# Performance work log

Hardware: AMD Instinct MI355X
Metric: run time of the kernel (lower is better)

Reference implementation:

```python
import jax, jax.numpy as jnp
import numpy as np

DIM = 256
NUM_HEADS = 4
HEAD_DIM = DIM // NUM_HEADS
MLP_HIDDEN = int(DIM * 2.0)
SCALE = HEAD_DIM ** -0.5
LN_EPS = 1e-5


def _layernorm(x, gamma, beta):
    mu = jnp.mean(x, axis=-1, keepdims=True)
    var = jnp.mean(jnp.square(x - mu), axis=-1, keepdims=True)
    return (x - mu) * jax.lax.rsqrt(var + LN_EPS) * gamma + beta


def setup_inputs() -> dict:
    key = jax.random.key(0)
    ks = jax.random.split(key, 8)
    B, C, N, P = 8, DIM, 64, 256
    s = 0.02
    return {
        "x": jax.random.normal(ks[0], (B, C, N, P), dtype=jnp.float32),
        # torch Linear weights stored [out_features, in_features]
        "W_qkv": jax.random.normal(ks[1], (3 * DIM, DIM), dtype=jnp.float32) * s,
        "W_proj": jax.random.normal(ks[2], (DIM, DIM), dtype=jnp.float32) * s,
        "b_proj": jnp.zeros((DIM,), dtype=jnp.float32),
        "ln1_g": jnp.ones((DIM,), dtype=jnp.float32),
        "ln1_b": jnp.zeros((DIM,), dtype=jnp.float32),
        "ln2_g": jnp.ones((DIM,), dtype=jnp.float32),
        "ln2_b": jnp.zeros((DIM,), dtype=jnp.float32),
        "W_mlp1": jax.random.normal(ks[3], (MLP_HIDDEN, DIM), dtype=jnp.float32) * s,
        "b_mlp1": jnp.zeros((MLP_HIDDEN,), dtype=jnp.float32),
        "W_mlp2": jax.random.normal(ks[4], (DIM, MLP_HIDDEN), dtype=jnp.float32) * s,
        "b_mlp2": jnp.zeros((DIM,), dtype=jnp.float32),
    }


def reference(x, W_qkv, W_proj, b_proj, ln1_g, ln1_b, ln2_g, ln2_b,
              W_mlp1, b_mlp1, W_mlp2, b_mlp2):
    B, C, N, P = x.shape
    H, D = NUM_HEADS, HEAD_DIM
    # [B,C,N,P] -> [B*N, P, C]
    x_seq = jnp.transpose(x, (0, 2, 3, 1)).reshape(B * N, P, C)
    shortcut = x_seq

    h = _layernorm(x_seq, ln1_g, ln1_b)
    qkv = jnp.einsum('spc,oc->spo', h, W_qkv)              # [BN, P, 3C]
    qkv = qkv.reshape(B * N, P, 3, H, D)
    q = jnp.transpose(qkv[:, :, 0], (0, 2, 1, 3))          # [BN, H, P, D]
    k = jnp.transpose(qkv[:, :, 1], (0, 2, 1, 3))
    v = jnp.transpose(qkv[:, :, 2], (0, 2, 1, 3))

    attn = jnp.einsum('shpd,shqd->shpq', q, k) * SCALE     # [BN, H, P, P]
    attn = jax.nn.softmax(attn, axis=-1)
    o = jnp.einsum('shpq,shqd->shpd', attn, v)             # [BN, H, P, D]
    o = jnp.transpose(o, (0, 2, 1, 3)).reshape(B * N, P, C)
    o = jnp.einsum('spc,oc->spo', o, W_proj) + b_proj

    x_seq = shortcut + o

    h2 = _layernorm(x_seq, ln2_g, ln2_b)
    m = jnp.einsum('spc,oc->spo', h2, W_mlp1) + b_mlp1
    m = jax.nn.gelu(m, approximate=False)
    m = jnp.einsum('sph,oh->spo', m, W_mlp2) + b_mlp2
    x_seq = x_seq + m

    out = x_seq.reshape(B, N, P, C)
    return jnp.transpose(out, (0, 3, 1, 2))                # [B, C, N, P]
```

## Files before the change

### kernel.cpp

```cpp
#include <hip/hip_runtime.h>
#include <stdint.h>
#include <math.h>


#define DEV static __device__ __forceinline__

typedef __bf16 bf16x8 __attribute__((ext_vector_type(8)));
typedef float  f32x4  __attribute__((ext_vector_type(4)));

union B8 { bf16x8 v; uint4 q; uint32_t u[4]; uint16_t h[8]; };

DEV uint16_t f2bf(float f) {
  uint32_t u = __float_as_uint(f);
  return (uint16_t)((u + 0x7FFFu + ((u >> 16) & 1u)) >> 16);
}
DEV float bf2f(uint16_t h) { return __uint_as_float(((uint32_t)h) << 16); }
DEV uint32_t pk2(float a, float b) { return (uint32_t)f2bf(a) | ((uint32_t)f2bf(b) << 16); }

DEV f32x4 mfma16(const B8& a, const B8& b, f32x4 c) {
  return __builtin_amdgcn_mfma_f32_16x16x32_bf16(a.v, b.v, c, 0, 0, 0);
}

DEV uint32_t shfl_u(uint32_t v, int src) { return (uint32_t)__shfl((int)v, src, 64); }

DEV B8 mk(const uint32_t* w) {
  B8 x; x.u[0] = w[0]; x.u[1] = w[1]; x.u[2] = w[2]; x.u[3] = w[3]; return x;
}

DEV void xpose(const uint32_t* pk0, const uint32_t* pk1, int kd, int g, int r, uint32_t* out) {
  const int sA = 32 * (g & 1) + r;
  const int sB = sA + 16;
  const int tA = 2 * kd, tB = 2 * kd + 1;
  uint32_t a0 = shfl_u(pk0[tA], sA), b0 = shfl_u(pk0[tB], sA);
  uint32_t a1 = shfl_u(pk1[tA], sA), b1 = shfl_u(pk1[tB], sA);
  uint32_t a2 = shfl_u(pk0[tA], sB), b2 = shfl_u(pk0[tB], sB);
  uint32_t a3 = shfl_u(pk1[tA], sB), b3 = shfl_u(pk1[tB], sB);
  const bool hi = g >= 2;
  out[0] = hi ? b0 : a0;
  out[1] = hi ? b1 : a1;
  out[2] = hi ? b2 : a2;
  out[3] = hi ? b3 : a3;
}

__global__ void transformer_prep(const float* __restrict__ wqkv,
                                 const float* __restrict__ wproj,
                                 const float* __restrict__ w1,
                                 const float* __restrict__ w2,
                                 uint16_t* __restrict__ wbf) {
  int e = blockIdx.x * 256 + threadIdx.x;
  float v;
  if (e < 196608)      v = wqkv[e] * (e < 65536 ? 0.18033688011112042f : 1.0f);
  else if (e < 262144) v = wproj[e - 196608];
  else if (e < 393216) v = w1[e - 262144];
  else                 v = w2[e - 393216];
  wbf[e] = f2bf(v);
}

__global__ __launch_bounds__(512, 2) void transformer_k1(
    const float* __restrict__ x,
    const float* __restrict__ bproj,
    const float* __restrict__ ln1g, const float* __restrict__ ln1b,
    const float* __restrict__ ln2g, const float* __restrict__ ln2b,
    const uint16_t* __restrict__ wbf,
    uint16_t* __restrict__ h2,
    float* __restrict__ out) {
  __shared__ __attribute__((aligned(16))) uint8_t lds[163840];
  const int tid = threadIdx.x;
  const int lane = tid & 63;
  const int wv = tid >> 6;
  const int r = lane & 15;
  const int g = lane >> 4;
  const int s = blockIdx.x;
  const int bb = s >> 6, nn = s & 63;
  const float* xs = x + (size_t)bb * 4194304 + (size_t)nn * 256;
  float* outp = out + (size_t)bb * 4194304 + (size_t)nn * 256;
  const f32x4 fz = {0.f, 0.f, 0.f, 0.f};

  uint32_t hfrag[2][8][4];
  float s1[2] = {0.f, 0.f}, s2[2] = {0.f, 0.f};
#pragma unroll
  for (int ch = 0; ch < 4; ++ch) {
#pragma unroll
    for (int i = 0; i < 8; ++i) {
      int f = i * 512 + tid;
      int c = f >> 6;
      int p4 = (f & 63) << 2;
      f32x4 v = *(const f32x4*)(xs + (size_t)(ch * 64 + c) * 16384 + p4);
      *(f32x4*)(lds + (c * 264 + p4) * 4) = v;
    }
    __syncthreads();
#pragma unroll
    for (int rt = 0; rt < 2; ++rt) {
      int p = 32 * wv + 16 * rt + r;
#pragma unroll
      for (int ktl = 0; ktl < 2; ++ktl) {
        int cl0 = 32 * ktl + 8 * g;
        float v[8];
#pragma unroll
        for (int j = 0; j < 8; ++j) {
          v[j] = *(const float*)(lds + ((cl0 + j) * 264 + p) * 4);
          s1[rt] += v[j];
          s2[rt] += v[j] * v[j];
        }
#pragma unroll
        for (int w = 0; w < 4; ++w) hfrag[rt][2 * ch + ktl][w] = pk2(v[2 * w], v[2 * w + 1]);
      }
    }
    __syncthreads();
  }
  float mu[2], rs[2];
#pragma unroll
  for (int rt = 0; rt < 2; ++rt) {
    float a = s1[rt]; a += __shfl_xor(a, 16, 64); a += __shfl_xor(a, 32, 64);
    float b = s2[rt]; b += __shfl_xor(b, 16, 64); b += __shfl_xor(b, 32, 64);
    mu[rt] = a * (1.0f / 256.0f);
    float var = b * (1.0f / 256.0f) - mu[rt] * mu[rt];
    rs[rt] = rsqrtf(var + 1e-5f);
  }
#pragma unroll
  for (int kt = 0; kt < 8; ++kt) {
    int c0 = 32 * kt + 8 * g;
    f32x4 gA = *(const f32x4*)(ln1g + c0), gB = *(const f32x4*)(ln1g + c0 + 4);
    f32x4 bA = *(const f32x4*)(ln1b + c0), bB = *(const f32x4*)(ln1b + c0 + 4);
#pragma unroll
    for (int rt = 0; rt < 2; ++rt) {
#pragma unroll
      for (int w = 0; w < 4; ++w) {
        uint32_t pw = hfrag[rt][kt][w];
        float lo = bf2f((uint16_t)(pw & 0xFFFFu));
        float hi = bf2f((uint16_t)(pw >> 16));
        float glo = (w < 2) ? gA[2 * w] : gB[2 * w - 4];
        float ghi = (w < 2) ? gA[2 * w + 1] : gB[2 * w - 3];
        float blo = (w < 2) ? bA[2 * w] : bB[2 * w - 4];
        float bhi = (w < 2) ? bA[2 * w + 1] : bB[2 * w - 3];
        lo = (lo - mu[rt]) * rs[rt] * glo + blo;
        hi = (hi - mu[rt]) * rs[rt] * ghi + bhi;
        hfrag[rt][kt][w] = pk2(lo, hi);
      }
    }
  }
  __syncthreads();

  uint32_t oa[2][8][4];
#pragma unroll
  for (int hd = 0; hd < 4; ++hd) {
#pragma unroll
    for (int m = 0; m < 3; ++m) {
      const uint16_t* src = wbf + (m * 256 + hd * 64) * 256;
#pragma unroll
      for (int i = 0; i < 4; ++i) {
        int f = i * 512 + tid;
        int row = f >> 5, c16 = f & 31;
        uint4 v = *(const uint4*)(src + row * 256 + c16 * 8);
        *(uint4*)(lds + ((65536 + m * 32768 + row * 512 + c16 * 16) ^ ((row & 7) << 4))) = v;
      }
    }
    __syncthreads();

#pragma unroll
    for (int m = 0; m < 2; ++m) {
      const int wb_base = 65536 + (m + 1) * 32768;
      f32x4 acc[2][4];
#pragma unroll
      for (int rt = 0; rt < 2; ++rt)
#pragma unroll
        for (int ct = 0; ct < 4; ++ct) acc[rt][ct] = fz;
#pragma unroll
      for (int kt = 0; kt < 8; ++kt) {
#pragma unroll
        for (int ct = 0; ct < 4; ++ct) {
          B8 wfr;
          wfr.q = *(const uint4*)(lds + ((wb_base + (16 * ct + r) * 512 + (32 * kt + 8 * g) * 2) ^ ((r & 7) << 4)));
#pragma unroll
          for (int rt = 0; rt < 2; ++rt) {
            B8 a = mk(hfrag[rt][kt]);
            acc[rt][ct] = mfma16(a, wfr, acc[rt][ct]);
          }
        }
      }
#pragma unroll
      for (int rt = 0; rt < 2; ++rt) {
#pragma unroll
        for (int ct = 0; ct < 4; ++ct) {
          int d = 16 * ct + r;
          int q0 = 32 * wv + 16 * rt + 4 * g;
          if (m == 0) {
#pragma unroll
            for (int i = 0; i < 4; ++i) {
              int qq = q0 + i;
              *(uint16_t*)(lds + ((qq * 128 + d * 2) ^ ((qq & 7) << 4))) = f2bf(acc[rt][ct][i]);
            }
          } else {
            uint2 pv;
            pv.x = pk2(acc[rt][ct][0], acc[rt][ct][1]);
            pv.y = pk2(acc[rt][ct][2], acc[rt][ct][3]);
            *(uint2*)(lds + ((32768 + d * 512 + q0 * 2) ^ ((d & 7) << 4))) = pv;
          }
        }
      }
    }
    __syncthreads();

#pragma unroll
    for (int pt = 0; pt < 2; ++pt) {
      f32x4 qT[4];
#pragma unroll
      for (int mt = 0; mt < 4; ++mt) qT[mt] = fz;
#pragma unroll
      for (int kt = 0; kt < 8; ++kt) {
        B8 hb = mk(hfrag[pt][kt]);
#pragma unroll
        for (int mt = 0; mt < 4; ++mt) {
          B8 wa;
          wa.q = *(const uint4*)(lds + ((65536 + (16 * mt + r) * 512 + (32 * kt + 8 * g) * 2) ^ ((r & 7) << 4)));
          qT[mt] = mfma16(wa, hb, qT[mt]);
        }
      }
      uint32_t pq0[4], pq1[4];
#pragma unroll
      for (int mt = 0; mt < 4; ++mt) {
        pq0[mt] = pk2(qT[mt][0], qT[mt][1]);
        pq1[mt] = pk2(qT[mt][2], qT[mt][3]);
      }
      uint32_t qb[2][4];
#pragma unroll
      for (int kd = 0; kd < 2; ++kd) xpose(pq0, pq1, kd, g, r, qb[kd]);

      float m_ = -1e30f, l_ = 0.f;
      f32x4 oT[4];
#pragma unroll
      for (int dt = 0; dt < 4; ++dt) oT[dt] = fz;

#pragma unroll 1
      for (int chk = 0; chk < 4; ++chk) {
        f32x4 sT[4];
#pragma unroll
        for (int qt = 0; qt < 4; ++qt) sT[qt] = fz;
#pragma unroll
        for (int kd = 0; kd < 2; ++kd) {
          B8 qf = mk(qb[kd]);
#pragma unroll
          for (int qt = 0; qt < 4; ++qt) {
            int qq = chk * 64 + 16 * qt + r;
            B8 ka;
            ka.q = *(const uint4*)(lds + ((qq * 128 + (32 * kd + 8 * g) * 2) ^ ((qq & 7) << 4)));
            sT[qt] = mfma16(ka, qf, sT[qt]);
          }
        }
        float tmax = sT[0][0];
#pragma unroll
        for (int qt = 0; qt < 4; ++qt)
#pragma unroll
          for (int i = 0; i < 4; ++i) tmax = fmaxf(tmax, sT[qt][i]);
        tmax = fmaxf(tmax, __shfl_xor(tmax, 16, 64));
        tmax = fmaxf(tmax, __shfl_xor(tmax, 32, 64));
        float mn = fmaxf(m_, tmax);
        float fcor = exp2f(m_ - mn);
        float ts = 0.f;
#pragma unroll
        for (int qt = 0; qt < 4; ++qt)
#pragma unroll
          for (int i = 0; i < 4; ++i) {
            float e = exp2f(sT[qt][i] - mn);
            sT[qt][i] = e;
            ts += e;
          }
        ts += __shfl_xor(ts, 16, 64);
        ts += __shfl_xor(ts, 32, 64);
        l_ = l_ * fcor + ts;
        m_ = mn;
#pragma unroll
        for (int dt = 0; dt < 4; ++dt)
#pragma unroll
          for (int i = 0; i < 4; ++i) oT[dt][i] *= fcor;
        uint32_t pp0[4], pp1[4];
#pragma unroll
        for (int qt = 0; qt < 4; ++qt) {
          pp0[qt] = pk2(sT[qt][0], sT[qt][1]);
          pp1[qt] = pk2(sT[qt][2], sT[qt][3]);
        }
#pragma unroll
        for (int qk = 0; qk < 2; ++qk) {
          uint32_t pb[4];
          xpose(pp0, pp1, qk, g, r, pb);
          B8 pf = mk(pb);
#pragma unroll
          for (int dt = 0; dt < 4; ++dt) {
            B8 va;
            va.q = *(const uint4*)(lds + ((32768 + (16 * dt + r) * 512 + (chk * 64 + 32 * qk + 8 * g) * 2) ^ ((r & 7) << 4)));
            oT[dt] = mfma16(va, pf, oT[dt]);
          }
        }
      }
      float inv = 1.0f / l_;
      uint32_t po0[4], po1[4];
#pragma unroll
      for (int dt = 0; dt < 4; ++dt) {
        po0[dt] = pk2(oT[dt][0] * inv, oT[dt][1] * inv);
        po1[dt] = pk2(oT[dt][2] * inv, oT[dt][3] * inv);
      }
#pragma unroll
      for (int kd = 0; kd < 2; ++kd) xpose(po0, po1, kd, g, r, oa[pt][2 * hd + kd]);
    }
    __syncthreads();
  }

  const uint16_t* wp = wbf + 196608;
  float s1r[2][4], s2r[2][4];
#pragma unroll
  for (int rt = 0; rt < 2; ++rt)
#pragma unroll
    for (int i = 0; i < 4; ++i) { s1r[rt][i] = 0.f; s2r[rt][i] = 0.f; }
#pragma unroll 1
  for (int q3 = 0; q3 < 4; ++q3) {
#pragma unroll
    for (int i = 0; i < 4; ++i) {
      int f = i * 512 + tid;
      int row = f >> 5, c16 = f & 31;
      uint4 v = *(const uint4*)(wp + (q3 * 64 + row) * 256 + c16 * 8);
      *(uint4*)(lds + ((131072 + row * 512 + c16 * 16) ^ ((row & 7) << 4))) = v;
    }
    __syncthreads();
    f32x4 acc[2][4];
#pragma unroll
    for (int rt = 0; rt < 2; ++rt)
#pragma unroll
      for (int ct = 0; ct < 4; ++ct) acc[rt][ct] = fz;
#pragma unroll
    for (int kt = 0; kt < 8; ++kt) {
#pragma unroll
      for (int ct = 0; ct < 4; ++ct) {
        B8 wfr;
        wfr.q = *(const uint4*)(lds + ((131072 + (16 * ct + r) * 512 + (32 * kt + 8 * g) * 2) ^ ((r & 7) << 4)));
#pragma unroll
        for (int rt = 0; rt < 2; ++rt) {
          B8 a = mk(oa[rt][kt]);
          acc[rt][ct] = mfma16(a, wfr, acc[rt][ct]);
        }
      }
    }
#pragma unroll
    for (int rt = 0; rt < 2; ++rt) {
#pragma unroll
      for (int ct = 0; ct < 4; ++ct) {
        int c = q3 * 64 + 16 * ct + r;
        float bias = bproj[c];
        int p0 = 32 * wv + 16 * rt + 4 * g;
        f32x4 res = *(const f32x4*)(xs + (size_t)c * 16384 + p0);
        f32x4 x2v;
#pragma unroll
        for (int i = 0; i < 4; ++i) x2v[i] = acc[rt][ct][i] + bias + res[i];
        *(f32x4*)(outp + (size_t)c * 16384 + p0) = x2v;
#pragma unroll
        for (int i = 0; i < 4; ++i) {
          s1r[rt][i] += x2v[i];
          s2r[rt][i] += x2v[i] * x2v[i];
          int pp = p0 + i;
          *(uint16_t*)(lds + ((pp * 512 + c * 2) ^ ((pp & 7) << 4))) = f2bf(x2v[i]);
        }
      }
    }
    __syncthreads();
  }
#pragma unroll
  for (int rt = 0; rt < 2; ++rt)
#pragma unroll
    for (int i = 0; i < 4; ++i) {
      float a = s1r[rt][i], b = s2r[rt][i];
#pragma unroll
      for (int off = 1; off < 16; off <<= 1) {
        a += __shfl_xor(a, off, 64);
        b += __shfl_xor(b, off, 64);
      }
      float m = a * (1.0f / 256.0f);
      float var = b * (1.0f / 256.0f) - m * m;
      s1r[rt][i] = m;
      s2r[rt][i] = rsqrtf(var + 1e-5f);
    }
  if (r == 0) {
#pragma unroll
    for (int rt = 0; rt < 2; ++rt)
#pragma unroll
      for (int i = 0; i < 4; ++i) {
        int pp = 32 * wv + 16 * rt + 4 * g + i;
        float2 st; st.x = s1r[rt][i]; st.y = s2r[rt][i];
        *(float2*)(lds + 131072 + pp * 8) = st;
      }
  }
  __syncthreads();
  {
    int pp = tid >> 1;
    int chf = tid & 1;
    float2 st = *(const float2*)(lds + 131072 + pp * 8);
#pragma unroll
    for (int kk = 0; kk < 16; ++kk) {
      int c0 = chf * 128 + kk * 8;
      B8 xv;
      xv.q = *(const uint4*)(lds + ((pp * 512 + c0 * 2) ^ ((pp & 7) << 4)));
      f32x4 gA = *(const f32x4*)(ln2g + c0), gB = *(const f32x4*)(ln2g + c0 + 4);
      f32x4 bA = *(const f32x4*)(ln2b + c0), bB = *(const f32x4*)(ln2b + c0 + 4);
      B8 ov;
#pragma unroll
      for (int j = 0; j < 8; ++j) {
        float v = bf2f(xv.h[j]);
        float gg = (j < 4) ? gA[j & 3] : gB[j & 3];
        float bb2 = (j < 4) ? bA[j & 3] : bB[j & 3];
        v = (v - st.x) * st.y * gg + bb2;
        ov.h[j] = f2bf(v);
      }
      *(uint4*)(h2 + (size_t)s * 65536 + pp * 256 + c0) = ov.q;
    }
  }
}

__global__ __launch_bounds__(512, 2) void transformer_k2(
    const uint16_t* __restrict__ h2,
    const uint16_t* __restrict__ w1,
    const uint16_t* __restrict__ w2,
    const float* __restrict__ bm1,
    const float* __restrict__ bm2,
    float* __restrict__ out) {
  __shared__ __attribute__((aligned(16))) uint8_t lds[98304];
  const int tid = threadIdx.x;
  const int lane = tid & 63;
  const int wv = tid >> 6;
  const int r = lane & 15, g = lane >> 4;
  const int bid = blockIdx.x;
  const int s = bid >> 2, tg = bid & 3;
  const int bb = s >> 6, nn = s & 63;
  const f32x4 fz = {0.f, 0.f, 0.f, 0.f};

#pragma unroll
  for (int i = 0; i < 4; ++i) {
    int f = i * 512 + tid;
    int row = f >> 5, c16 = f & 31;
    uint4 v = *(const uint4*)(h2 + (size_t)s * 65536 + (tg * 64 + row) * 256 + c16 * 8);
    *(uint4*)(lds + ((row * 512 + c16 * 16) ^ ((row & 7) << 4))) = v;
  }
  __syncthreads();

  f32x4 acc[4][4];
#pragma unroll
  for (int mt = 0; mt < 4; ++mt)
#pragma unroll
    for (int nt = 0; nt < 4; ++nt) acc[mt][nt] = fz;
#pragma unroll
  for (int kt = 0; kt < 8; ++kt) {
    B8 a[4];
#pragma unroll
    for (int mt = 0; mt < 4; ++mt)
      a[mt].q = *(const uint4*)(lds + (((16 * mt + r) * 512 + (32 * kt + 8 * g) * 2) ^ ((r & 7) << 4)));
#pragma unroll
    for (int nt = 0; nt < 4; ++nt) {
      B8 bfr;
      bfr.q = *(const uint4*)(w1 + ((64 * wv + 16 * nt + r) * 256 + 32 * kt + 8 * g));
#pragma unroll
      for (int mt = 0; mt < 4; ++mt) acc[mt][nt] = mfma16(a[mt], bfr, acc[mt][nt]);
    }
  }
#pragma unroll
  for (int nt = 0; nt < 4; ++nt) {
    int n = 64 * wv + 16 * nt + r;
    float bias = bm1[n];
#pragma unroll
    for (int mt = 0; mt < 4; ++mt) {
#pragma unroll
      for (int i = 0; i < 4; ++i) {
        float v = acc[mt][nt][i] + bias;
        v = 0.5f * v * (1.0f + erff(v * 0.70710678118654752440f));
        int row = 16 * mt + 4 * g + i;
        *(uint16_t*)(lds + ((32768 + row * 1024 + n * 2) ^ ((row & 7) << 4))) = f2bf(v);
      }
    }
  }
  __syncthreads();

  f32x4 acc2[4][2];
#pragma unroll
  for (int mt = 0; mt < 4; ++mt)
#pragma unroll
    for (int nt = 0; nt < 2; ++nt) acc2[mt][nt] = fz;
#pragma unroll
  for (int kt = 0; kt < 16; ++kt) {
    B8 a[4];
#pragma unroll
    for (int mt = 0; mt < 4; ++mt)
      a[mt].q = *(const uint4*)(lds + ((32768 + (16 * mt + r) * 1024 + (32 * kt + 8 * g) * 2) ^ ((r & 7) << 4)));
#pragma unroll
    for (int nt = 0; nt < 2; ++nt) {
      B8 bfr;
      bfr.q = *(const uint4*)(w2 + ((32 * wv + 16 * nt + r) * 512 + 32 * kt + 8 * g));
#pragma unroll
      for (int mt = 0; mt < 4; ++mt) acc2[mt][nt] = mfma16(a[mt], bfr, acc2[mt][nt]);
    }
  }
  float* outp = out + (size_t)bb * 4194304 + (size_t)nn * 256;
#pragma unroll
  for (int nt = 0; nt < 2; ++nt) {
    int c = 32 * wv + 16 * nt + r;
    float bias = bm2[c];
#pragma unroll
    for (int mt = 0; mt < 4; ++mt) {
      int p0 = tg * 64 + 16 * mt + 4 * g;
      f32x4 v = *(const f32x4*)(outp + (size_t)c * 16384 + p0);
#pragma unroll
      for (int i = 0; i < 4; ++i) v[i] += acc2[mt][nt][i] + bias;
      *(f32x4*)(outp + (size_t)c * 16384 + p0) = v;
    }
  }
}

extern "C" void kernel_launch(void* const* d_in, const int* in_sizes, int n_in,
                              void* d_out, int out_size, void* d_ws, size_t ws_size,
                              hipStream_t stream) {
  (void)in_sizes; (void)n_in; (void)out_size; (void)ws_size;
  const float* x     = (const float*)d_in[0];
  const float* wqkv  = (const float*)d_in[1];
  const float* wproj = (const float*)d_in[2];
  const float* bproj = (const float*)d_in[3];
  const float* ln1g  = (const float*)d_in[4];
  const float* ln1b  = (const float*)d_in[5];
  const float* ln2g  = (const float*)d_in[6];
  const float* ln2b  = (const float*)d_in[7];
  const float* w1    = (const float*)d_in[8];
  const float* bm1   = (const float*)d_in[9];
  const float* w2    = (const float*)d_in[10];
  const float* bm2   = (const float*)d_in[11];
  uint16_t* wbf = (uint16_t*)d_ws;
  uint16_t* h2  = wbf + 524288;
  float* out = (float*)d_out;

  transformer_prep<<<2048, 256, 0, stream>>>(wqkv, wproj, w1, w2, wbf);
  transformer_k1<<<512, 512, 0, stream>>>(x, bproj, ln1g, ln1b, ln2g, ln2b, wbf, h2, out);
  transformer_k2<<<2048, 512, 0, stream>>>(h2, wbf + 262144, wbf + 393216, bm1, bm2, out);
}
```

Baseline: 779.7 us.

## Pre-swizzle weights into MFMA fragment order, shrink LDS, move LN2 into MLP kernel

The prep kernel now writes bf16 weights in MFMA fragment-tiled order, so both kernels read weight fragments straight from global memory instead of staging them through LDS. Kernel 1 drops from 160KB to 64KB of LDS with launch bounds raised to 4 blocks, reads x directly from global, and spills attention output fragments to a workspace instead of holding them in registers. LayerNorm2 moves from kernel 1 into kernel 2, which recomputes statistics from the residual stream it reads back. The MLP is split into two hidden halves to cut register and LDS use. The cost is more global traffic: strided uncoalesced x reads, repeated weight fragment loads from cache, and an extra osc round trip.

After: 1.049 ms. +34.6%, slower.

```diff
diff --git a/kernel.cpp b/kernel.cpp
--- a/kernel.cpp
+++ b/kernel.cpp
@@ -46,25 +46,31 @@
                                  const float* __restrict__ wproj,
                                  const float* __restrict__ w1,
                                  const float* __restrict__ w2,
-                                 uint16_t* __restrict__ wbf) {
+                                 uint16_t* __restrict__ dst) {
   int e = blockIdx.x * 256 + threadIdx.x;
-  float v;
-  if (e < 196608)      v = wqkv[e] * (e < 65536 ? 0.18033688011112042f : 1.0f);
-  else if (e < 262144) v = wproj[e - 196608];
-  else if (e < 393216) v = w1[e - 262144];
-  else                 v = w2[e - 393216];
-  wbf[e] = f2bf(v);
-}
-
-__global__ __launch_bounds__(512, 2) void transformer_k1(
+  const float* src; int C, local;
+  if (e < 196608)      { src = wqkv;  C = 256; local = e; }
+  else if (e < 262144) { src = wproj; C = 256; local = e - 196608; }
+  else if (e < 393216) { src = w1;    C = 256; local = e - 262144; }
+  else                 { src = w2;    C = 512; local = e - 393216; }
+  int k32 = C >> 5;
+  int tile = local >> 9, within = local & 511;
+  int ln = within >> 3, j = within & 7;
+  int tr = tile / k32, tk = tile - tr * k32;
+  int row = tr * 16 + (ln & 15), col = tk * 32 + (ln >> 4) * 8 + j;
+  float v = src[row * C + col];
+  if (e < 65536) v *= 0.18033688011112042f;
+  dst[e] = f2bf(v);
+}
+
+__global__ __launch_bounds__(512, 4) void transformer_k1(
     const float* __restrict__ x,
     const float* __restrict__ bproj,
     const float* __restrict__ ln1g, const float* __restrict__ ln1b,
-    const float* __restrict__ ln2g, const float* __restrict__ ln2b,
-    const uint16_t* __restrict__ wbf,
-    uint16_t* __restrict__ h2,
+    const uint16_t* __restrict__ wf,
+    uint16_t* __restrict__ osc,
     float* __restrict__ out) {
-  __shared__ __attribute__((aligned(16))) uint8_t lds[163840];
+  __shared__ __attribute__((aligned(16))) uint8_t lds[65536];
   const int tid = threadIdx.x;
   const int lane = tid & 63;
   const int wv = tid >> 6;
@@ -79,34 +85,21 @@
   uint32_t hfrag[2][8][4];
   float s1[2] = {0.f, 0.f}, s2[2] = {0.f, 0.f};
 #pragma unroll
-  for (int ch = 0; ch < 4; ++ch) {
-#pragma unroll
-    for (int i = 0; i < 8; ++i) {
-      int f = i * 512 + tid;
-      int c = f >> 6;
-      int p4 = (f & 63) << 2;
-      f32x4 v = *(const f32x4*)(xs + (size_t)(ch * 64 + c) * 16384 + p4);
-      *(f32x4*)(lds + (c * 264 + p4) * 4) = v;
-    }
-    __syncthreads();
-#pragma unroll
-    for (int rt = 0; rt < 2; ++rt) {
-      int p = 32 * wv + 16 * rt + r;
-#pragma unroll
-      for (int ktl = 0; ktl < 2; ++ktl) {
-        int cl0 = 32 * ktl + 8 * g;
-        float v[8];
-#pragma unroll
-        for (int j = 0; j < 8; ++j) {
-          v[j] = *(const float*)(lds + ((cl0 + j) * 264 + p) * 4);
-          s1[rt] += v[j];
-          s2[rt] += v[j] * v[j];
-        }
-#pragma unroll
-        for (int w = 0; w < 4; ++w) hfrag[rt][2 * ch + ktl][w] = pk2(v[2 * w], v[2 * w + 1]);
-      }
-    }
-    __syncthreads();
+  for (int rt = 0; rt < 2; ++rt) {
+    int p = 32 * wv + 16 * rt + r;
+#pragma unroll
+    for (int kt = 0; kt < 8; ++kt) {
+      int c0 = 32 * kt + 8 * g;
+      float v[8];
+#pragma unroll
+      for (int j = 0; j < 8; ++j) {
+        v[j] = xs[(size_t)(c0 + j) * 16384 + p];
+        s1[rt] += v[j];
+        s2[rt] += v[j] * v[j];
+      }
+#pragma unroll
+      for (int w = 0; w < 4; ++w) hfrag[rt][kt][w] = pk2(v[2 * w], v[2 * w + 1]);
+    }
   }
   float mu[2], rs[2];
 #pragma unroll
@@ -139,27 +132,11 @@
       }
     }
   }
-  __syncthreads();
-
-  uint32_t oa[2][8][4];
-#pragma unroll
+
+#pragma unroll 1
   for (int hd = 0; hd < 4; ++hd) {
 #pragma unroll
-    for (int m = 0; m < 3; ++m) {
-      const uint16_t* src = wbf + (m * 256 + hd * 64) * 256;
-#pragma unroll
-      for (int i = 0; i < 4; ++i) {
-        int f = i * 512 + tid;
-        int row = f >> 5, c16 = f & 31;
-        uint4 v = *(const uint4*)(src + row * 256 + c16 * 8);
-        *(uint4*)(lds + ((65536 + m * 32768 + row * 512 + c16 * 16) ^ ((row & 7) << 4))) = v;
-      }
-    }
-    __syncthreads();
-
-#pragma unroll
     for (int m = 0; m < 2; ++m) {
-      const int wb_base = 65536 + (m + 1) * 32768;
       f32x4 acc[2][4];
 #pragma unroll
       for (int rt = 0; rt < 2; ++rt)
@@ -170,7 +147,7 @@
 #pragma unroll
         for (int ct = 0; ct < 4; ++ct) {
           B8 wfr;
-          wfr.q = *(const uint4*)(lds + ((wb_base + (16 * ct + r) * 512 + (32 * kt + 8 * g) * 2) ^ ((r & 7) << 4)));
+          wfr.q = *(const uint4*)(wf + (size_t)((((m + 1) * 16 + hd * 4 + ct) * 8 + kt) * 512) + lane * 8);
 #pragma unroll
           for (int rt = 0; rt < 2; ++rt) {
             B8 a = mk(hfrag[rt][kt]);
@@ -201,7 +178,7 @@
     }
     __syncthreads();
 
-#pragma unroll
+#pragma unroll 1
     for (int pt = 0; pt < 2; ++pt) {
       f32x4 qT[4];
 #pragma unroll
@@ -212,7 +189,7 @@
 #pragma unroll
         for (int mt = 0; mt < 4; ++mt) {
           B8 wa;
-          wa.q = *(const uint4*)(lds + ((65536 + (16 * mt + r) * 512 + (32 * kt + 8 * g) * 2) ^ ((r & 7) << 4)));
+          wa.q = *(const uint4*)(wf + (size_t)(((hd * 4 + mt) * 8 + kt) * 512) + lane * 8);
           qT[mt] = mfma16(wa, hb, qT[mt]);
         }
       }
@@ -300,27 +277,18 @@
         po1[dt] = pk2(oT[dt][2] * inv, oT[dt][3] * inv);
       }
 #pragma unroll
-      for (int kd = 0; kd < 2; ++kd) xpose(po0, po1, kd, g, r, oa[pt][2 * hd + kd]);
+      for (int kd = 0; kd < 2; ++kd) {
+        uint32_t ofr[4];
+        xpose(po0, po1, kd, g, r, ofr);
+        B8 t; t.u[0] = ofr[0]; t.u[1] = ofr[1]; t.u[2] = ofr[2]; t.u[3] = ofr[3];
+        *(uint4*)(osc + (size_t)((s * 16 + 2 * wv + pt) * 8 + 2 * hd + kd) * 512 + lane * 8) = t.q;
+      }
     }
     __syncthreads();
   }
 
-  const uint16_t* wp = wbf + 196608;
-  float s1r[2][4], s2r[2][4];
-#pragma unroll
-  for (int rt = 0; rt < 2; ++rt)
-#pragma unroll
-    for (int i = 0; i < 4; ++i) { s1r[rt][i] = 0.f; s2r[rt][i] = 0.f; }
 #pragma unroll 1
   for (int q3 = 0; q3 < 4; ++q3) {
-#pragma unroll
-    for (int i = 0; i < 4; ++i) {
-      int f = i * 512 + tid;
-      int row = f >> 5, c16 = f & 31;
-      uint4 v = *(const uint4*)(wp + (q3 * 64 + row) * 256 + c16 * 8);
-      *(uint4*)(lds + ((131072 + row * 512 + c16 * 16) ^ ((row & 7) << 4))) = v;
-    }
-    __syncthreads();
     f32x4 acc[2][4];
 #pragma unroll
     for (int rt = 0; rt < 2; ++rt)
@@ -328,15 +296,16 @@
       for (int ct = 0; ct < 4; ++ct) acc[rt][ct] = fz;
 #pragma unroll
     for (int kt = 0; kt < 8; ++kt) {
+      B8 a[2];
+#pragma unroll
+      for (int rt = 0; rt < 2; ++rt)
+        a[rt].q = *(const uint4*)(osc + (size_t)((s * 16 + 2 * wv + rt) * 8 + kt) * 512 + lane * 8);
 #pragma unroll
       for (int ct = 0; ct < 4; ++ct) {
         B8 wfr;
-        wfr.q = *(const uint4*)(lds + ((131072 + (16 * ct + r) * 512 + (32 * kt + 8 * g) * 2) ^ ((r & 7) << 4)));
-#pragma unroll
-        for (int rt = 0; rt < 2; ++rt) {
-          B8 a = mk(oa[rt][kt]);
-          acc[rt][ct] = mfma16(a, wfr, acc[rt][ct]);
-        }
+        wfr.q = *(const uint4*)(wf + 196608 + (size_t)(((q3 * 4 + ct) * 8 + kt) * 512) + lane * 8);
+#pragma unroll
+        for (int rt = 0; rt < 2; ++rt) acc[rt][ct] = mfma16(a[rt], wfr, acc[rt][ct]);
       }
     }
 #pragma unroll
@@ -351,76 +320,17 @@
 #pragma unroll
         for (int i = 0; i < 4; ++i) x2v[i] = acc[rt][ct][i] + bias + res[i];
         *(f32x4*)(outp + (size_t)c * 16384 + p0) = x2v;
-#pragma unroll
-        for (int i = 0; i < 4; ++i) {
-          s1r[rt][i] += x2v[i];
-          s2r[rt][i] += x2v[i] * x2v[i];
-          int pp = p0 + i;
-          *(uint16_t*)(lds + ((pp * 512 + c * 2) ^ ((pp & 7) << 4))) = f2bf(x2v[i]);
-        }
-      }
-    }
-    __syncthreads();
-  }
-#pragma unroll
-  for (int rt = 0; rt < 2; ++rt)
-#pragma unroll
-    for (int i = 0; i < 4; ++i) {
-      float a = s1r[rt][i], b = s2r[rt][i];
-#pragma unroll
-      for (int off = 1; off < 16; off <<= 1) {
-        a += __shfl_xor(a, off, 64);
-        b += __shfl_xor(b, off, 64);
-      }
-      float m = a * (1.0f / 256.0f);
-      float var = b * (1.0f / 256.0f) - m * m;
-      s1r[rt][i] = m;
-      s2r[rt][i] = rsqrtf(var + 1e-5f);
-    }
-  if (r == 0) {
-#pragma unroll
-    for (int rt = 0; rt < 2; ++rt)
-#pragma unroll
-      for (int i = 0; i < 4; ++i) {
-        int pp = 32 * wv + 16 * rt + 4 * g + i;
-        float2 st; st.x = s1r[rt][i]; st.y = s2r[rt][i];
-        *(float2*)(lds + 131072 + pp * 8) = st;
-      }
-  }
-  __syncthreads();
-  {
-    int pp = tid >> 1;
-    int chf = tid & 1;
-    float2 st = *(const float2*)(lds + 131072 + pp * 8);
-#pragma unroll
-    for (int kk = 0; kk < 16; ++kk) {
-      int c0 = chf * 128 + kk * 8;
-      B8 xv;
-      xv.q = *(const uint4*)(lds + ((pp * 512 + c0 * 2) ^ ((pp & 7) << 4)));
-      f32x4 gA = *(const f32x4*)(ln2g + c0), gB = *(const f32x4*)(ln2g + c0 + 4);
-      f32x4 bA = *(const f32x4*)(ln2b + c0), bB = *(const f32x4*)(ln2b + c0 + 4);
-      B8 ov;
-#pragma unroll
-      for (int j = 0; j < 8; ++j) {
-        float v = bf2f(xv.h[j]);
-        float gg = (j < 4) ? gA[j & 3] : gB[j & 3];
-        float bb2 = (j < 4) ? bA[j & 3] : bB[j & 3];
-        v = (v - st.x) * st.y * gg + bb2;
-        ov.h[j] = f2bf(v);
-      }
-      *(uint4*)(h2 + (size_t)s * 65536 + pp * 256 + c0) = ov.q;
-    }
-  }
-}
-
-__global__ __launch_bounds__(512, 2) void transformer_k2(
-    const uint16_t* __restrict__ h2,
-    const uint16_t* __restrict__ w1,
-    const uint16_t* __restrict__ w2,
-    const float* __restrict__ bm1,
-    const float* __restrict__ bm2,
+      }
+    }
+  }
+}
+
+__global__ __launch_bounds__(512, 4) void transformer_k2(
+    const float* __restrict__ ln2g, const float* __restrict__ ln2b,
+    const uint16_t* __restrict__ w1f, const uint16_t* __restrict__ w2f,
+    const float* __restrict__ bm1, const float* __restrict__ bm2,
     float* __restrict__ out) {
-  __shared__ __attribute__((aligned(16))) uint8_t lds[98304];
+  __shared__ __attribute__((aligned(16))) uint8_t lds[68608];
   const int tid = threadIdx.x;
   const int lane = tid & 63;
   const int wv = tid >> 6;
@@ -428,84 +338,135 @@
   const int bid = blockIdx.x;
   const int s = bid >> 2, tg = bid & 3;
   const int bb = s >> 6, nn = s & 63;
+  float* outp = out + (size_t)bb * 4194304 + (size_t)nn * 256;
+  const int tokbase = tg * 64;
   const f32x4 fz = {0.f, 0.f, 0.f, 0.f};
-
-#pragma unroll
-  for (int i = 0; i < 4; ++i) {
-    int f = i * 512 + tid;
-    int row = f >> 5, c16 = f & 31;
-    uint4 v = *(const uint4*)(h2 + (size_t)s * 65536 + (tg * 64 + row) * 256 + c16 * 8);
-    *(uint4*)(lds + ((row * 512 + c16 * 16) ^ ((row & 7) << 4))) = v;
+  const int mtw = wv & 3, kth = wv >> 2;
+  const int p = tokbase + 16 * mtw + r;
+
+  float v[4][8];
+  float s1 = 0.f, s2 = 0.f;
+#pragma unroll
+  for (int k2l = 0; k2l < 4; ++k2l) {
+    int c0 = (kth * 4 + k2l) * 32 + 8 * g;
+#pragma unroll
+    for (int j = 0; j < 8; ++j) {
+      float t = outp[(size_t)(c0 + j) * 16384 + p];
+      v[k2l][j] = t;
+      s1 += t;
+      s2 += t * t;
+    }
+  }
+  s1 += __shfl_xor(s1, 16, 64); s1 += __shfl_xor(s1, 32, 64);
+  s2 += __shfl_xor(s2, 16, 64); s2 += __shfl_xor(s2, 32, 64);
+  if (g == 0) {
+    float2 pr; pr.x = s1; pr.y = s2;
+    *(float2*)(lds + 65536 + ((16 * mtw + r) * 2 + kth) * 8) = pr;
   }
   __syncthreads();
-
-  f32x4 acc[4][4];
+  if (tid < 64) {
+    float2 a = *(const float2*)(lds + 65536 + (tid * 2 + 0) * 8);
+    float2 b = *(const float2*)(lds + 65536 + (tid * 2 + 1) * 8);
+    float su = a.x + b.x, sq = a.y + b.y;
+    float m = su * (1.0f / 256.0f);
+    float var = sq * (1.0f / 256.0f) - m * m;
+    float2 st; st.x = m; st.y = rsqrtf(var + 1e-5f);
+    *(float2*)(lds + 66560 + tid * 8) = st;
+  }
+  __syncthreads();
+  float2 st = *(const float2*)(lds + 66560 + (16 * mtw + r) * 8);
+#pragma unroll
+  for (int k2l = 0; k2l < 4; ++k2l) {
+    int kt = kth * 4 + k2l;
+    int c0 = kt * 32 + 8 * g;
+    f32x4 gA = *(const f32x4*)(ln2g + c0), gB = *(const f32x4*)(ln2g + c0 + 4);
+    f32x4 bA = *(const f32x4*)(ln2b + c0), bB = *(const f32x4*)(ln2b + c0 + 4);
+    float nv[8];
+#pragma unroll
+    for (int j = 0; j < 8; ++j) {
+      float gg = (j < 4) ? gA[j] : gB[j - 4];
+      float bb2 = (j < 4) ? bA[j] : bB[j - 4];
+      nv[j] = (v[k2l][j] - st.x) * st.y * gg + bb2;
+    }
+    B8 t;
+#pragma unroll
+    for (int w = 0; w < 4; ++w) t.u[w] = pk2(nv[2 * w], nv[2 * w + 1]);
+    *(uint4*)(lds + (mtw * 8 + kt) * 1024 + lane * 16) = t.q;
+  }
+  __syncthreads();
+
+  f32x4 acc2[4][2];
 #pragma unroll
   for (int mt = 0; mt < 4; ++mt)
 #pragma unroll
-    for (int nt = 0; nt < 4; ++nt) acc[mt][nt] = fz;
-#pragma unroll
-  for (int kt = 0; kt < 8; ++kt) {
-    B8 a[4];
+    for (int nt = 0; nt < 2; ++nt) acc2[mt][nt] = fz;
+
+#pragma unroll 1
+  for (int half = 0; half < 2; ++half) {
+    f32x4 acc1[4][2];
 #pragma unroll
     for (int mt = 0; mt < 4; ++mt)
-      a[mt].q = *(const uint4*)(lds + (((16 * mt + r) * 512 + (32 * kt + 8 * g) * 2) ^ ((r & 7) << 4)));
-#pragma unroll
-    for (int nt = 0; nt < 4; ++nt) {
-      B8 bfr;
-      bfr.q = *(const uint4*)(w1 + ((64 * wv + 16 * nt + r) * 256 + 32 * kt + 8 * g));
-#pragma unroll
-      for (int mt = 0; mt < 4; ++mt) acc[mt][nt] = mfma16(a[mt], bfr, acc[mt][nt]);
-    }
-  }
-#pragma unroll
-  for (int nt = 0; nt < 4; ++nt) {
-    int n = 64 * wv + 16 * nt + r;
-    float bias = bm1[n];
+#pragma unroll
+      for (int nt = 0; nt < 2; ++nt) acc1[mt][nt] = fz;
+#pragma unroll
+    for (int kt = 0; kt < 8; ++kt) {
+      B8 a[4];
+#pragma unroll
+      for (int mt = 0; mt < 4; ++mt)
+        a[mt].q = *(const uint4*)(lds + (mt * 8 + kt) * 1024 + lane * 16);
+#pragma unroll
+      for (int nt = 0; nt < 2; ++nt) {
+        B8 bfr;
+        bfr.q = *(const uint4*)(w1f + (size_t)((((half * 16 + wv * 2 + nt) * 8) + kt) * 512) + lane * 8);
+#pragma unroll
+        for (int mt = 0; mt < 4; ++mt) acc1[mt][nt] = mfma16(a[mt], bfr, acc1[mt][nt]);
+      }
+    }
+    if (half) __syncthreads();
+#pragma unroll
+    for (int nt = 0; nt < 2; ++nt) {
+      int nl = wv * 32 + 16 * nt + r;
+      float bias = bm1[half * 256 + nl];
+#pragma unroll
+      for (int mt = 0; mt < 4; ++mt) {
+#pragma unroll
+        for (int i = 0; i < 4; ++i) {
+          float vv = acc1[mt][nt][i] + bias;
+          vv = 0.5f * vv * (1.0f + erff(vv * 0.70710678118654752440f));
+          int lp = (4 * g + i) + 16 * ((nl >> 3) & 3);
+          *(uint16_t*)(lds + 32768 + (mt * 8 + wv) * 1024 + lp * 16 + (nl & 7) * 2) = f2bf(vv);
+        }
+      }
+    }
+    __syncthreads();
+#pragma unroll
+    for (int kt = 0; kt < 8; ++kt) {
+      B8 a[4];
+#pragma unroll
+      for (int mt = 0; mt < 4; ++mt)
+        a[mt].q = *(const uint4*)(lds + 32768 + (mt * 8 + kt) * 1024 + lane * 16);
+#pragma unroll
+      for (int nt = 0; nt < 2; ++nt) {
+        B8 bfr;
+        bfr.q = *(const uint4*)(w2f + (size_t)(((wv * 2 + nt) * 16 + half * 8 + kt) * 512) + lane * 8);
+#pragma unroll
+        for (int mt = 0; mt < 4; ++mt) acc2[mt][nt] = mfma16(a[mt], bfr, acc2[mt][nt]);
+      }
+    }
+  }
+
+#pragma unroll
+  for (int nt = 0; nt < 2; ++nt) {
+    int c = wv * 32 + 16 * nt + r;
+    float bias = bm2[c];
 #pragma unroll
     for (int mt = 0; mt < 4; ++mt) {
-#pragma unroll
-      for (int i = 0; i < 4; ++i) {
-        float v = acc[mt][nt][i] + bias;
-        v = 0.5f * v * (1.0f + erff(v * 0.70710678118654752440f));
-        int row = 16 * mt + 4 * g + i;
-        *(uint16_t*)(lds + ((32768 + row * 1024 + n * 2) ^ ((row & 7) << 4))) = f2bf(v);
-      }
-    }
-  }
-  __syncthreads();
-
-  f32x4 acc2[4][2];
-#pragma unroll
-  for (int mt = 0; mt < 4; ++mt)
-#pragma unroll
-    for (int nt = 0; nt < 2; ++nt) acc2[mt][nt] = fz;
-#pragma unroll
-  for (int kt = 0; kt < 16; ++kt) {
-    B8 a[4];
-#pragma unroll
-    for (int mt = 0; mt < 4; ++mt)
-      a[mt].q = *(const uint4*)(lds + ((32768 + (16 * mt + r) * 1024 + (32 * kt + 8 * g) * 2) ^ ((r & 7) << 4)));
-#pragma unroll
-    for (int nt = 0; nt < 2; ++nt) {
-      B8 bfr;
-      bfr.q = *(const uint4*)(w2 + ((32 * wv + 16 * nt + r) * 512 + 32 * kt + 8 * g));
-#pragma unroll
-      for (int mt = 0; mt < 4; ++mt) acc2[mt][nt] = mfma16(a[mt], bfr, acc2[mt][nt]);
-    }
-  }
-  float* outp = out + (size_t)bb * 4194304 + (size_t)nn * 256;
-#pragma unroll
-  for (int nt = 0; nt < 2; ++nt) {
-    int c = 32 * wv + 16 * nt + r;
-    float bias = bm2[c];
-#pragma unroll
-    for (int mt = 0; mt < 4; ++mt) {
-      int p0 = tg * 64 + 16 * mt + 4 * g;
-      f32x4 v = *(const f32x4*)(outp + (size_t)c * 16384 + p0);
-#pragma unroll
-      for (int i = 0; i < 4; ++i) v[i] += acc2[mt][nt][i] + bias;
-      *(f32x4*)(outp + (size_t)c * 16384 + p0) = v;
+      int p0 = tokbase + 16 * mt + 4 * g;
+      f32x4 res = *(const f32x4*)(outp + (size_t)c * 16384 + p0);
+      f32x4 o;
+#pragma unroll
+      for (int i = 0; i < 4; ++i) o[i] = res[i] + acc2[mt][nt][i] + bias;
+      *(f32x4*)(outp + (size_t)c * 16384 + p0) = o;
     }
   }
 }
@@ -527,10 +488,10 @@
   const float* w2    = (const float*)d_in[10];
   const float* bm2   = (const float*)d_in[11];
   uint16_t* wbf = (uint16_t*)d_ws;
-  uint16_t* h2  = wbf + 524288;
+  uint16_t* osc = wbf + 524288;
   float* out = (float*)d_out;
 
   transformer_prep<<<2048, 256, 0, stream>>>(wqkv, wproj, w1, w2, wbf);
-  transformer_k1<<<512, 512, 0, stream>>>(x, bproj, ln1g, ln1b, ln2g, ln2b, wbf, h2, out);
-  transformer_k2<<<2048, 512, 0, stream>>>(h2, wbf + 262144, wbf + 393216, bm1, bm2, out);
-}
+  transformer_k1<<<512, 512, 0, stream>>>(x, bproj, ln1g, ln1b, wbf, osc, out);
+  transformer_k2<<<2048, 512, 0, stream>>>(ln2g, ln2b, wbf + 262144, wbf + 393216, bm1, bm2, out);
+}
```
